# Optimization experiments

Measured on AMD Instinct MI355X. Metric: run time of the kernel, lower is better.

## Reference

```python
import jax, jax.numpy as jnp
import numpy as np
from jax import lax

EPS = 1e-5

def conv2d(x, w, pad):
    return lax.conv_general_dilated(x, w, (1, 1), [(pad, pad), (pad, pad)],
                                    dimension_numbers=('NCHW', 'OIHW', 'NCHW'))

def bn(x, g, b, m, v):
    scale = (g / jnp.sqrt(v + EPS))[None, :, None, None]
    return (x - m[None, :, None, None]) * scale + b[None, :, None, None]

def upsample_bilinear_align_corners(x, scale):
    b, c, h, w = x.shape
    oh, ow = h * scale, w * scale
    ys = jnp.linspace(0.0, h - 1.0, oh)
    xs = jnp.linspace(0.0, w - 1.0, ow)
    y0 = jnp.floor(ys).astype(jnp.int32); y1 = jnp.minimum(y0 + 1, h - 1)
    x0 = jnp.floor(xs).astype(jnp.int32); x1 = jnp.minimum(x0 + 1, w - 1)
    wy = (ys - y0)[None, None, :, None]
    wx = (xs - x0)[None, None, None, :]
    rows = x[:, :, y0, :] * (1.0 - wy) + x[:, :, y1, :] * wy   # (b,c,oh,w)
    return rows[:, :, :, x0] * (1.0 - wx) + rows[:, :, :, x1] * wx

def setup_inputs() -> dict:
    key = jax.random.key(0)
    ks = jax.random.split(key, 12)
    Cin, C4, C8, NC = 2048, 512, 256, 19
    B, H, W = 4, 32, 32
    s = lambda fan: 1.0 / np.sqrt(fan)
    inp = {
        'x': jax.random.normal(ks[0], (B, Cin, H, W), dtype=jnp.float32),
        'conv1_w': jax.random.normal(ks[1], (C4, Cin, 3, 3), jnp.float32) * s(Cin * 9),
        'bn1_g': jnp.ones((C4,)), 'bn1_b': jnp.zeros((C4,)),
        'bn1_m': jnp.zeros((C4,)), 'bn1_v': jnp.ones((C4,)),
        'conv2_w': jax.random.normal(ks[2], (C4, Cin, 3, 3), jnp.float32) * s(Cin * 9),
        'bn2_g': jnp.ones((C4,)), 'bn2_b': jnp.zeros((C4,)),
        'bn2_m': jnp.zeros((C4,)), 'bn2_v': jnp.ones((C4,)),
        'pa_convB_w': jax.random.normal(ks[3], (C4, C4, 1, 1), jnp.float32) * s(C4),
        'pa_gamma': jnp.zeros((1,)),
        'ca_beta': jnp.zeros((1,)),
        'conv3_w': jax.random.normal(ks[4], (C4, C4, 3, 3), jnp.float32) * s(C4 * 9),
        'bn3_g': jnp.ones((C4,)), 'bn3_b': jnp.zeros((C4,)),
        'bn3_m': jnp.zeros((C4,)), 'bn3_v': jnp.ones((C4,)),
        'conv4a_w': jax.random.normal(ks[5], (C8, C4, 3, 3), jnp.float32) * s(C4 * 9),
        'bn4_g': jnp.ones((C8,)), 'bn4_b': jnp.zeros((C8,)),
        'bn4_m': jnp.zeros((C8,)), 'bn4_v': jnp.ones((C8,)),
        'conv4b_w': jax.random.normal(ks[6], (NC, C8, 3, 3), jnp.float32) * s(C8 * 9),
    }
    return inp

def position_attention(x, convB_w, gamma):
    b, c, h, w = x.shape
    # NOTE: original code uses convB for B, C and D (convC/convD unused) - faithful.
    Bm = conv2d(x, convB_w, 0).reshape(b, c, h * w)          # (b,c,hw)
    S = jax.nn.softmax(jnp.einsum('bcn,bcm->bnm', Bm, Bm), axis=-1)  # (b,hw,hw)
    E = jnp.einsum('bcm,bnm->bcn', Bm, S).reshape(b, c, h, w)
    return gamma * E + x

def channel_attention(x, beta):
    b, c, h, w = x.shape
    xf = x.reshape(b, c, h * w)
    A = jax.nn.softmax(jnp.einsum('bcn,bdn->bcd', xf, xf), axis=-1)  # (b,c,c)
    X = jnp.einsum('bkc,bkn->bcn', A, xf).reshape(b, c, h, w)        # A^T @ xf
    return beta * X + x

def reference(x, conv1_w, bn1_g, bn1_b, bn1_m, bn1_v,
              conv2_w, bn2_g, bn2_b, bn2_m, bn2_v,
              pa_convB_w, pa_gamma, ca_beta,
              conv3_w, bn3_g, bn3_b, bn3_m, bn3_v,
              conv4a_w, bn4_g, bn4_b, bn4_m, bn4_v, conv4b_w):
    x_pa = jax.nn.relu(bn(conv2d(x, conv1_w, 1), bn1_g, bn1_b, bn1_m, bn1_v))
    x_ca = jax.nn.relu(bn(conv2d(x, conv2_w, 1), bn2_g, bn2_b, bn2_m, bn2_v))
    pa = position_attention(x_pa, pa_convB_w, pa_gamma)
    ca = channel_attention(x_ca, ca_beta)
    out = jax.nn.relu(bn(conv2d(pa + ca, conv3_w, 1), bn3_g, bn3_b, bn3_m, bn3_v))
    out = upsample_bilinear_align_corners(out, 8)
    out = jax.nn.relu(bn(conv2d(out, conv4a_w, 1), bn4_g, bn4_b, bn4_m, bn4_v))
    out = conv2d(out, conv4b_w, 1)
    return out
```

## Files before the change

### kernel.cpp

```cpp
#include <hip/hip_runtime.h>
#include <stdint.h>

typedef __bf16 v8bf __attribute__((ext_vector_type(8)));
typedef float  v4f  __attribute__((ext_vector_type(4)));

#define MFMA16(a,b,c) __builtin_amdgcn_mfma_f32_16x16x32_bf16((a),(b),(c),0,0,0)

__device__ __forceinline__ void g2l16(void* lds, const void* g) {
  __builtin_amdgcn_global_load_lds(
      (__attribute__((address_space(1))) unsigned int*)g,
      (__attribute__((address_space(3))) unsigned int*)lds, 16, 0, 0);
}


__global__ void bnprep(const float* __restrict__ g, const float* __restrict__ b,
                       const float* __restrict__ m, const float* __restrict__ v,
                       float* __restrict__ sc, float* __restrict__ bi, int C) {
  int i = blockIdx.x * 256 + threadIdx.x;
  if (i < C) {
    float s = g[i] * rsqrtf(v[i] + 1e-5f);
    sc[i] = s;
    bi[i] = b[i] - m[i] * s;
  }
}

__global__ void pack_w(const float* __restrict__ src, __bf16* __restrict__ dst,
                       int co_cnt, int co_src, int co_off, int co_tot, int ci, int taps) {
  int idx = blockIdx.x * 256 + threadIdx.x;
  if (idx >= co_cnt * ci) return;
  int c = idx % ci, co = idx / ci;
  for (int t = 0; t < taps; ++t) {
    float v = (co < co_src) ? src[((size_t)co * ci + c) * taps + t] : 0.f;
    dst[((size_t)t * co_tot + co_off + co) * ci + c] = (__bf16)v;
  }
}

__global__ void cast_x_k(const float* __restrict__ x, __bf16* __restrict__ xb) {
  __shared__ float tl[64][65];
  int p0 = blockIdx.x * 64, c0 = blockIdx.y * 64, n = blockIdx.z;
  const float* xin = x + (size_t)n * 2048 * 1024;
  for (int it = 0; it < 16; ++it) {
    int idx = it * 256 + threadIdx.x;
    int px = idx & 63, cl = idx >> 6;
    tl[px][cl] = xin[(size_t)(c0 + cl) * 1024 + p0 + px];
  }
  __syncthreads();
  for (int it = 0; it < 16; ++it) {
    int idx = it * 256 + threadIdx.x;
    int cl = idx & 63, px = idx >> 6;
    xb[((size_t)n * 1024 + p0 + px) * 2048 + c0 + cl] = (__bf16)tl[px][cl];
  }
}

__global__ void trans_y2(const __bf16* __restrict__ y12, __bf16* __restrict__ y2t) {
  __shared__ __bf16 tl[64][72];
  int p0 = blockIdx.x * 64, c0 = blockIdx.y * 64, n = blockIdx.z;
  for (int it = 0; it < 16; ++it) {
    int idx = it * 256 + threadIdx.x;
    int cl = idx & 63, px = idx >> 6;
    tl[px][cl] = y12[((size_t)n * 1024 + p0 + px) * 1024 + 512 + c0 + cl];
  }
  __syncthreads();
  for (int it = 0; it < 16; ++it) {
    int idx = it * 256 + threadIdx.x;
    int px = idx & 63, cl = idx >> 6;
    y2t[((size_t)n * 512 + c0 + cl) * 1024 + p0 + px] = tl[px][cl];
  }
}

__global__ __launch_bounds__(256, 2)
void gemm_nt(const __bf16* __restrict__ A, const __bf16* __restrict__ B,
             size_t aB, size_t bB, int lda, int ldb, int kch, int mode,
             void* __restrict__ out, void* __restrict__ out2, size_t oB, int ldo) {
  __shared__ __align__(16) __bf16 tile[2][4 * 128 * 8];
  const int tid = threadIdx.x;
  const int lane = tid & 63, wv = tid >> 6;
  const int ln = lane & 15, q = lane >> 4;
  const int wm = wv >> 1, wn = wv & 1;
  const int p0 = blockIdx.x * 128, mb = blockIdx.y * 128, z = blockIdx.z;
  A += (size_t)z * aB; B += (size_t)z * bB;

  v4f acc[4][4];
#pragma unroll
  for (int mf = 0; mf < 4; ++mf)
#pragma unroll
    for (int nf = 0; nf < 4; ++nf)
#pragma unroll
      for (int r = 0; r < 4; ++r) acc[mf][nf][r] = 0.f;

  const __bf16* pa[4];
#pragma unroll
  for (int mf = 0; mf < 4; ++mf)
    pa[mf] = A + (size_t)(mb + wm * 64 + mf * 16 + ln) * lda + q * 8;

#pragma unroll
  for (int t2 = 0; t2 < 2; ++t2)
    g2l16(&tile[0][(wv * 128 + t2 * 64) * 8],
          B + (size_t)(p0 + t2 * 64 + lane) * ldb + wv * 8);
  __syncthreads();

  for (int kc = 0; kc < kch; ++kc) {
    const int tb = kc & 1;
    if (kc + 1 < kch) {
      const int c1 = (kc + 1) * 32;
#pragma unroll
      for (int t2 = 0; t2 < 2; ++t2)
        g2l16(&tile[tb ^ 1][(wv * 128 + t2 * 64) * 8],
              B + (size_t)(p0 + t2 * 64 + lane) * ldb + c1 + wv * 8);
    }
    const int c0 = kc * 32;
    v8bf bfr[4];
#pragma unroll
    for (int nf = 0; nf < 4; ++nf)
      bfr[nf] = *(const v8bf*)&tile[tb][(q * 128 + wn * 64 + nf * 16 + ln) * 8];
#pragma unroll
    for (int mf = 0; mf < 4; ++mf) {
      v8bf af = *(const v8bf*)(pa[mf] + c0);
#pragma unroll
      for (int nf = 0; nf < 4; ++nf)
        acc[mf][nf] = MFMA16(af, bfr[nf], acc[mf][nf]);
    }
    __syncthreads();
  }

#pragma unroll
  for (int mf = 0; mf < 4; ++mf) {
    const int m_l = wm * 64 + mf * 16 + q * 4;
#pragma unroll
    for (int nf = 0; nf < 4; ++nf) {
      const int n_l = wn * 64 + nf * 16 + ln;
      const int P = p0 + n_l;
      if (mode == 1) {
        float* o = (float*)out + (size_t)z * oB;
#pragma unroll
        for (int r = 0; r < 4; ++r)
          o[(size_t)(mb + m_l + r) * ldo + P] = acc[mf][nf][r];
      } else if (mode == 3) {
        float* o = (float*)out + (size_t)z * oB;
        v4f v;
#pragma unroll
        for (int r = 0; r < 4; ++r) v[r] = acc[mf][nf][r];
        *(v4f*)(o + (size_t)P * ldo + mb + m_l) = v;
      } else {
        __bf16* o = (__bf16*)out + (size_t)z * oB;
        union { __bf16 h[4]; uint2 u; } pk;
#pragma unroll
        for (int r = 0; r < 4; ++r) pk.h[r] = (__bf16)acc[mf][nf][r];
        *(uint2*)(o + (size_t)P * ldo + mb + m_l) = pk.u;
        if (mode == 2) {
          __bf16* o2 = (__bf16*)out2 + (size_t)z * oB;
#pragma unroll
          for (int r = 0; r < 4; ++r)
            o2[(size_t)(mb + m_l + r) * 1024 + P] = pk.h[r];
        }
      }
    }
  }
}

template <int CI, int KCH, int KS>
__global__ __launch_bounds__(256, 4)
void conv3x3_sk(const __bf16* __restrict__ in, const __bf16* __restrict__ wp,
                float* __restrict__ part, const int CO) {
  __shared__ __align__(16) __bf16 tile[2][816 * 8];
  const int tid = threadIdx.x;
  const int lane = tid & 63, wv = tid >> 6;
  const int ln = lane & 15, q = lane >> 4;
  const int pblk = blockIdx.x, cb = blockIdx.y, ks = blockIdx.z;
  const int n = pblk >> 3, y0 = (pblk & 7) << 2;
  const int wm = wv >> 1, wn = wv & 1;
  const int KCN = KCH / KS;
  const int kbase = ks * KCN;

  for (int t = tid; t < 1632; t += 256) ((uint4*)tile)[t] = make_uint4(0, 0, 0, 0);

  v4f acc[4][4];
#pragma unroll
  for (int mf = 0; mf < 4; ++mf)
#pragma unroll
    for (int nf = 0; nf < 4; ++nf)
#pragma unroll
      for (int r = 0; r < 4; ++r) acc[mf][nf][r] = 0.f;

  const __bf16* pa[4];
#pragma unroll
  for (int mf = 0; mf < 4; ++mf) {
    int co = cb * 128 + wm * 64 + mf * 16 + ln;
    pa[mf] = wp + (size_t)co * CI + kbase * 32 + q * 8;
  }
  int pixb[4];
#pragma unroll
  for (int nf = 0; nf < 4; ++nf) {
    int n_l = wn * 64 + nf * 16 + ln;
    pixb[nf] = (n_l >> 5) * 34 + (n_l & 31);
  }
  const __bf16* inb = in + (size_t)n * 1024 * CI + kbase * 32;
  __syncthreads();

  if (lane < 32) {
#pragma unroll
    for (int t2 = 0; t2 < 6; ++t2) {
      int y = y0 - 1 + t2;
      if (y >= 0 && y < 32)
        g2l16(&tile[0][(wv * 204 + t2 * 34 + 1) * 8],
              inb + ((size_t)(y * 32 + lane) * CI + wv * 8));
    }
  }
  __syncthreads();

  for (int kc = 0; kc < KCN; ++kc) {
    const int tb = kc & 1;
    if (kc + 1 < KCN && lane < 32) {
      const int c1 = (kc + 1) * 32;
#pragma unroll
      for (int t2 = 0; t2 < 6; ++t2) {
        int y = y0 - 1 + t2;
        if (y >= 0 && y < 32)
          g2l16(&tile[tb ^ 1][(wv * 204 + t2 * 34 + 1) * 8],
                inb + ((size_t)(y * 32 + lane) * CI + c1 + wv * 8));
      }
    }
    const int ci0 = kc * 32;
#pragma unroll
    for (int tap = 0; tap < 9; ++tap) {
      const int ty = tap / 3, tx = tap % 3;
      v8bf bfr[4];
#pragma unroll
      for (int nf = 0; nf < 4; ++nf)
        bfr[nf] = *(const v8bf*)&tile[tb][(q * 204 + pixb[nf] + ty * 34 + tx) * 8];
      const size_t toff = (size_t)tap * CO * CI + ci0;
#pragma unroll
      for (int mf = 0; mf < 4; ++mf) {
        v8bf af = *(const v8bf*)(pa[mf] + toff);
#pragma unroll
        for (int nf = 0; nf < 4; ++nf)
          acc[mf][nf] = MFMA16(af, bfr[nf], acc[mf][nf]);
      }
    }
    __syncthreads();
  }

  float* po = part + ((size_t)ks * 4096 + (size_t)n * 1024) * CO;
#pragma unroll
  for (int mf = 0; mf < 4; ++mf) {
    const int m_l = wm * 64 + mf * 16 + q * 4;
#pragma unroll
    for (int nf = 0; nf < 4; ++nf) {
      const int n_l = wn * 64 + nf * 16 + ln;
      const int p_img = (y0 + (n_l >> 5)) * 32 + (n_l & 31);
      *(v4f*)(po + (size_t)p_img * CO + cb * 128 + m_l) = acc[mf][nf];
    }
  }
}

template <int CO, int KS>
__global__ __launch_bounds__(256, 8)
void reduce_bn_relu(const float* __restrict__ part, const float* __restrict__ sc,
                    const float* __restrict__ bi, __bf16* __restrict__ out) {
  const size_t splitStride = (size_t)4096 * CO;
  size_t gi = (size_t)blockIdx.x * 256 + threadIdx.x;
  size_t row = gi / (CO / 4);
  int c4 = (int)(gi % (CO / 4)) * 4;
  const float* p = part + row * CO + c4;
  v4f a = *(const v4f*)p;
#pragma unroll
  for (int s = 1; s < KS; ++s) {
    v4f b = *(const v4f*)(p + s * splitStride);
#pragma unroll
    for (int r = 0; r < 4; ++r) a[r] += b[r];
  }
  const v4f s4 = *(const v4f*)(sc + c4);
  const v4f b4 = *(const v4f*)(bi + c4);
  union { __bf16 h[4]; uint2 u; } pk;
#pragma unroll
  for (int r = 0; r < 4; ++r)
    pk.h[r] = (__bf16)fmaxf(a[r] * s4[r] + b4[r], 0.f);
  *(uint2*)(out + row * CO + c4) = pk.u;
}

__global__ __launch_bounds__(256, 4)
void up_combine(const float* __restrict__ D, const float* __restrict__ sc,
                const float* __restrict__ bi, __bf16* __restrict__ y4) {
  const int tid = threadIdx.x;
  const int coq = blockIdx.x;
  const int oy = blockIdx.y;
  const int n = blockIdx.z;
  const int co = coq * 64 + (tid & 15) * 4;
  const int px0 = (tid >> 4) * 16;

  const v4f s4 = *(const v4f*)(sc + co);
  const v4f b4 = *(const v4f*)(bi + co);

  v4f acc[16];
#pragma unroll
  for (int j = 0; j < 16; ++j)
#pragma unroll
    for (int r = 0; r < 4; ++r) acc[j][r] = 0.f;

  const float* Dn = D + (size_t)n * 1024 * 2304;

#pragma unroll
  for (int ty = 0; ty < 3; ++ty) {
    int fy = oy + ty - 1;
    if (fy < 0 || fy > 255) continue;
    float syf = fy * (31.0f / 255.0f);
    int rA = (int)syf; float wy = syf - rA;
    int rB = rA < 31 ? rA + 1 : 31;
    float wA = 1.f - wy, wB = wy;
    const float* rowA = Dn + (size_t)rA * 32 * 2304;
    const float* rowB = Dn + (size_t)rB * 32 * 2304;
#pragma unroll
    for (int tx = 0; tx < 3; ++tx) {
      const int tco = (ty * 3 + tx) * 256 + co;
      int cur = -99;
      v4f a0{}, a1{}, b0{}, b1{};
#pragma unroll
      for (int j = 0; j < 16; ++j) {
        int fx = px0 + j + tx - 1;
        if (fx < 0 || fx > 255) continue;
        float sxf = fx * (31.0f / 255.0f);
        int c0 = (int)sxf; float wx = sxf - c0;
        if (c0 != cur) {
          cur = c0;
          int c1 = c0 < 31 ? c0 + 1 : 31;
          a0 = *(const v4f*)(rowA + (size_t)c0 * 2304 + tco);
          a1 = *(const v4f*)(rowA + (size_t)c1 * 2304 + tco);
          b0 = *(const v4f*)(rowB + (size_t)c0 * 2304 + tco);
          b1 = *(const v4f*)(rowB + (size_t)c1 * 2304 + tco);
        }
        float wxA = 1.f - wx;
        float cA = wA * wxA, cB = wA * wx, cC = wB * wxA, cD = wB * wx;
#pragma unroll
        for (int r = 0; r < 4; ++r)
          acc[j][r] += cA * a0[r] + cB * a1[r] + cC * b0[r] + cD * b1[r];
      }
    }
  }

  __bf16* ob = y4 + (((size_t)n * 65536 + (size_t)oy * 256 + px0) * 256 + co);
#pragma unroll
  for (int j = 0; j < 16; ++j) {
    union { __bf16 h[4]; uint2 u; } pk;
#pragma unroll
    for (int r = 0; r < 4; ++r) {
      float v = acc[j][r] * s4[r] + b4[r];
      pk.h[r] = (__bf16)fmaxf(v, 0.f);
    }
    *(uint2*)(ob + (size_t)j * 256) = pk.u;
  }
}

__global__ __launch_bounds__(256, 4)
void conv4b_k(const __bf16* __restrict__ y4, const __bf16* __restrict__ wp,
              float* __restrict__ outp) {
  __shared__ __align__(16) __bf16 tile[2][816 * 8];
  const int tid = threadIdx.x;
  const int lane = tid & 63, wv = tid >> 6;
  const int ln = lane & 15, q = lane >> 4;
  const int xblk = blockIdx.x, strip = blockIdx.y, n = blockIdx.z;
  const int oy0 = strip * 4, ox0 = xblk * 32;

  for (int t = tid; t < 1632; t += 256) ((uint4*)tile)[t] = make_uint4(0, 0, 0, 0);

  v4f acc[2][2];
#pragma unroll
  for (int mf = 0; mf < 2; ++mf)
#pragma unroll
    for (int nf = 0; nf < 2; ++nf)
#pragma unroll
      for (int r = 0; r < 4; ++r) acc[mf][nf][r] = 0.f;

  const __bf16* pa[2];
#pragma unroll
  for (int mf = 0; mf < 2; ++mf)
    pa[mf] = wp + (size_t)(mf * 16 + ln) * 256 + q * 8;
  int pixb[2];
#pragma unroll
  for (int nf = 0; nf < 2; ++nf) {
    int n_l = wv * 32 + nf * 16 + ln;
    pixb[nf] = (n_l >> 5) * 34 + (n_l & 31);
  }
  const __bf16* src = y4 + (size_t)n * 65536 * 256;
  const int gx = ox0 - 1 + lane;
  const bool xin = (lane < 34) && (gx >= 0) && (gx < 256);
  __syncthreads();

#pragma unroll
  for (int t2 = 0; t2 < 6; ++t2) {
    int y = oy0 - 1 + t2;
    if (y >= 0 && y < 256 && xin)
      g2l16(&tile[0][(wv * 204 + t2 * 34) * 8],
            src + ((size_t)(y * 256 + gx) * 256 + wv * 8));
  }
  __syncthreads();

  for (int kc = 0; kc < 8; ++kc) {
    const int tb = kc & 1;
    if (kc + 1 < 8) {
      const int c1 = (kc + 1) * 32;
#pragma unroll
      for (int t2 = 0; t2 < 6; ++t2) {
        int y = oy0 - 1 + t2;
        if (y >= 0 && y < 256 && xin)
          g2l16(&tile[tb ^ 1][(wv * 204 + t2 * 34) * 8],
                src + ((size_t)(y * 256 + gx) * 256 + c1 + wv * 8));
      }
    }
    const int ci0 = kc * 32;
#pragma unroll
    for (int tap = 0; tap < 9; ++tap) {
      const int ty = tap / 3, tx = tap % 3;
      v8bf bfr[2];
#pragma unroll
      for (int nf = 0; nf < 2; ++nf)
        bfr[nf] = *(const v8bf*)&tile[tb][(q * 204 + pixb[nf] + ty * 34 + tx) * 8];
      const size_t toff = (size_t)tap * 32 * 256 + ci0;
#pragma unroll
      for (int mf = 0; mf < 2; ++mf) {
        v8bf af = *(const v8bf*)(pa[mf] + toff);
#pragma unroll
        for (int nf = 0; nf < 2; ++nf)
          acc[mf][nf] = MFMA16(af, bfr[nf], acc[mf][nf]);
      }
    }
    __syncthreads();
  }

#pragma unroll
  for (int mf = 0; mf < 2; ++mf) {
    const int m_l = mf * 16 + q * 4;
#pragma unroll
    for (int nf = 0; nf < 2; ++nf) {
      const int n_l = wv * 32 + nf * 16 + ln;
      const int oy = oy0 + (n_l >> 5), ox = ox0 + (n_l & 31);
#pragma unroll
      for (int r = 0; r < 4; ++r) {
        int co = m_l + r;
        if (co < 19)
          outp[(((size_t)n * 19 + co) * 256 + oy) * 256 + ox] = acc[mf][nf][r];
      }
    }
  }
}


__global__ void softmax1024(const float* __restrict__ S, __bf16* __restrict__ O) {
  __shared__ float red[256];
  const int row = blockIdx.x, tid = threadIdx.x;
  const float* p = S + (size_t)row * 1024;
  float v0 = p[tid], v1 = p[tid + 256], v2 = p[tid + 512], v3 = p[tid + 768];
  float m = fmaxf(fmaxf(v0, v1), fmaxf(v2, v3));
  red[tid] = m; __syncthreads();
  for (int s = 128; s > 0; s >>= 1) { if (tid < s) red[tid] = fmaxf(red[tid], red[tid + s]); __syncthreads(); }
  m = red[0]; __syncthreads();
  v0 = __expf(v0 - m); v1 = __expf(v1 - m); v2 = __expf(v2 - m); v3 = __expf(v3 - m);
  red[tid] = v0 + v1 + v2 + v3; __syncthreads();
  for (int s = 128; s > 0; s >>= 1) { if (tid < s) red[tid] += red[tid + s]; __syncthreads(); }
  float inv = 1.0f / red[0];
  __bf16* o = O + (size_t)row * 1024;
  o[tid] = (__bf16)(v0 * inv); o[tid + 256] = (__bf16)(v1 * inv);
  o[tid + 512] = (__bf16)(v2 * inv); o[tid + 768] = (__bf16)(v3 * inv);
}

__global__ void softmaxT512(const float* __restrict__ S, __bf16* __restrict__ O) {
  __shared__ float red[256];
  const int row = blockIdx.x, tid = threadIdx.x;
  const float* p = S + (size_t)row * 512;
  float v0 = p[tid], v1 = p[tid + 256];
  float m = fmaxf(v0, v1);
  red[tid] = m; __syncthreads();
  for (int s = 128; s > 0; s >>= 1) { if (tid < s) red[tid] = fmaxf(red[tid], red[tid + s]); __syncthreads(); }
  m = red[0]; __syncthreads();
  v0 = __expf(v0 - m); v1 = __expf(v1 - m);
  red[tid] = v0 + v1; __syncthreads();
  for (int s = 128; s > 0; s >>= 1) { if (tid < s) red[tid] += red[tid + s]; __syncthreads(); }
  float inv = 1.0f / red[0];
  int n = row >> 9, c = row & 511;
  __bf16* o = O + (size_t)n * 262144 + c;
  o[(size_t)tid * 512] = (__bf16)(v0 * inv);
  o[(size_t)(tid + 256) * 512] = (__bf16)(v1 * inv);
}

__global__ void combine_z(const __bf16* __restrict__ y12, const __bf16* __restrict__ E,
                          const __bf16* __restrict__ X, const float* __restrict__ gp,
                          const float* __restrict__ bp, __bf16* __restrict__ z) {
  size_t i = (size_t)blockIdx.x * 256 + threadIdx.x;
  int pg = (int)(i >> 9), c = (int)(i & 511);
  float g = gp[0], b = bp[0];
  float v = (float)y12[(size_t)pg * 1024 + c] + (float)y12[(size_t)pg * 1024 + 512 + c] +
            g * (float)E[i] + b * (float)X[i];
  z[i] = (__bf16)v;
}


extern "C" void kernel_launch(void* const* d_in, const int* in_sizes, int n_in,
                              void* d_out, int out_size, void* d_ws, size_t ws_size,
                              hipStream_t stream) {
  const float* x    = (const float*)d_in[0];
  const float* w1   = (const float*)d_in[1];
  const float* bn1g = (const float*)d_in[2];
  const float* bn1b = (const float*)d_in[3];
  const float* bn1m = (const float*)d_in[4];
  const float* bn1v = (const float*)d_in[5];
  const float* w2   = (const float*)d_in[6];
  const float* bn2g = (const float*)d_in[7];
  const float* bn2b = (const float*)d_in[8];
  const float* bn2m = (const float*)d_in[9];
  const float* bn2v = (const float*)d_in[10];
  const float* wB   = (const float*)d_in[11];
  const float* gam  = (const float*)d_in[12];
  const float* bet  = (const float*)d_in[13];
  const float* w3   = (const float*)d_in[14];
  const float* bn3g = (const float*)d_in[15];
  const float* bn3b = (const float*)d_in[16];
  const float* bn3m = (const float*)d_in[17];
  const float* bn3v = (const float*)d_in[18];
  const float* w4a  = (const float*)d_in[19];
  const float* bn4g = (const float*)d_in[20];
  const float* bn4b = (const float*)d_in[21];
  const float* bn4m = (const float*)d_in[22];
  const float* bn4v = (const float*)d_in[23];
  const float* w4b  = (const float*)d_in[24];

  char* ws = (char*)d_ws;
  size_t off = 0;
  auto take = [&](size_t bytes) -> char* {
    char* p = ws + off;
    off += (bytes + 255) & ~(size_t)255;
    return p;
  };
  __bf16* w12b  = (__bf16*)take(9ULL * 1024 * 2048 * 2);
  __bf16* w3b   = (__bf16*)take(9ULL * 512 * 512 * 2);
  __bf16* w4ab  = (__bf16*)take(9ULL * 256 * 512 * 2);
  __bf16* w4bb  = (__bf16*)take(9ULL * 32 * 256 * 2);
  __bf16* wBb   = (__bf16*)take(512ULL * 512 * 2);
  float*  sc12  = (float*)take(1024 * 4);
  float*  bi12  = (float*)take(1024 * 4);
  float*  sc3   = (float*)take(512 * 4);
  float*  bi3   = (float*)take(512 * 4);
  float*  sc4   = (float*)take(256 * 4);
  float*  bi4   = (float*)take(256 * 4);
  __bf16* xb    = (__bf16*)take(4ULL * 1024 * 2048 * 2);
  __bf16* y12   = (__bf16*)take(4ULL * 1024 * 1024 * 2);
  __bf16* Bm_pc = (__bf16*)take(4ULL * 1024 * 512 * 2);
  __bf16* Bm_cp = (__bf16*)take(4ULL * 512 * 1024 * 2);
  float*  Smat  = (float*)take(4ULL * 1024 * 1024 * 4);
  __bf16* Ssm   = (__bf16*)take(4ULL * 1024 * 1024 * 2);
  __bf16* E_pc  = (__bf16*)take(4ULL * 1024 * 512 * 2);
  __bf16* y2t   = (__bf16*)take(4ULL * 512 * 1024 * 2);
  float*  Scc   = (float*)take(4ULL * 512 * 512 * 4);
  __bf16* AsmT  = (__bf16*)take(4ULL * 512 * 512 * 2);
  __bf16* X_pc  = (__bf16*)take(4ULL * 1024 * 512 * 2);
  __bf16* zb    = (__bf16*)take(4ULL * 1024 * 512 * 2);
  __bf16* y4    = (__bf16*)take(4ULL * 65536 * 256 * 2);
  __bf16* y3    = (__bf16*)take(4ULL * 1024 * 512 * 2);
  float* Dmat = (float*)xb;
  float* partK = (float*)y4;

  bnprep<<<2, 256, 0, stream>>>(bn1g, bn1b, bn1m, bn1v, sc12, bi12, 512);
  bnprep<<<2, 256, 0, stream>>>(bn2g, bn2b, bn2m, bn2v, sc12 + 512, bi12 + 512, 512);
  bnprep<<<2, 256, 0, stream>>>(bn3g, bn3b, bn3m, bn3v, sc3, bi3, 512);
  bnprep<<<1, 256, 0, stream>>>(bn4g, bn4b, bn4m, bn4v, sc4, bi4, 256);
  pack_w<<<4096, 256, 0, stream>>>(w1, w12b, 512, 512, 0, 1024, 2048, 9);
  pack_w<<<4096, 256, 0, stream>>>(w2, w12b, 512, 512, 512, 1024, 2048, 9);
  pack_w<<<1024, 256, 0, stream>>>(w3, w3b, 512, 512, 0, 512, 512, 9);
  pack_w<<<512, 256, 0, stream>>>(w4a, w4ab, 256, 256, 0, 256, 512, 9);
  pack_w<<<32, 256, 0, stream>>>(w4b, w4bb, 32, 19, 0, 32, 256, 9);
  pack_w<<<1024, 256, 0, stream>>>(wB, wBb, 512, 512, 0, 512, 512, 1);
  cast_x_k<<<dim3(16, 32, 4), 256, 0, stream>>>(x, xb);

  conv3x3_sk<2048, 64, 4><<<dim3(32, 8, 4), 256, 0, stream>>>(xb, w12b, partK, 1024);
  reduce_bn_relu<1024, 4><<<4096, 256, 0, stream>>>(partK, sc12, bi12, y12);

  gemm_nt<<<dim3(8, 4, 4), 256, 0, stream>>>(wBb, y12, 0, 1048576, 512, 1024, 16, 2,
                                             Bm_pc, Bm_cp, 524288, 512);
  gemm_nt<<<dim3(8, 8, 4), 256, 0, stream>>>(Bm_pc, Bm_pc, 524288, 524288, 512, 512, 16, 1,
                                             Smat, nullptr, 1048576, 1024);
  softmax1024<<<4096, 256, 0, stream>>>(Smat, Ssm);
  gemm_nt<<<dim3(8, 4, 4), 256, 0, stream>>>(Bm_cp, Ssm, 524288, 1048576, 1024, 1024, 32, 0,
                                             E_pc, nullptr, 524288, 512);

  trans_y2<<<dim3(16, 8, 4), 256, 0, stream>>>(y12, y2t);
  gemm_nt<<<dim3(4, 4, 4), 256, 0, stream>>>(y2t, y2t, 524288, 524288, 1024, 1024, 32, 1,
                                             Scc, nullptr, 262144, 512);
  softmaxT512<<<2048, 256, 0, stream>>>(Scc, AsmT);
  gemm_nt<<<dim3(8, 4, 4), 256, 0, stream>>>(AsmT, y12 + 512, 262144, 1048576, 512, 1024, 16, 0,
                                             X_pc, nullptr, 524288, 512);

  combine_z<<<8192, 256, 0, stream>>>(y12, E_pc, X_pc, gam, bet, zb);

  conv3x3_sk<512, 16, 4><<<dim3(32, 4, 4), 256, 0, stream>>>(zb, w3b, partK, 512);
  reduce_bn_relu<512, 4><<<2048, 256, 0, stream>>>(partK, sc3, bi3, y3);

  gemm_nt<<<dim3(8, 18, 4), 256, 0, stream>>>(w4ab, y3, 0, 524288, 512, 512, 16, 3,
                                              Dmat, nullptr, 2359296, 2304);
  up_combine<<<dim3(4, 256, 4), 256, 0, stream>>>(Dmat, sc4, bi4, y4);

  conv4b_k<<<dim3(8, 64, 4), 256, 0, stream>>>(y4, w4bb, (float*)d_out);
}
```

Baseline: 1.301 ms.

## Register-prefetch weight fragments in conv and GEMM loops; reorder conv grid

```diff
diff --git a/kernel.cpp b/kernel.cpp
--- a/kernel.cpp
+++ b/kernel.cpp
@@ -97,6 +97,9 @@
   for (int t2 = 0; t2 < 2; ++t2)
     g2l16(&tile[0][(wv * 128 + t2 * 64) * 8],
           B + (size_t)(p0 + t2 * 64 + lane) * ldb + wv * 8);
+  v8bf acur[4];
+#pragma unroll
+  for (int mf = 0; mf < 4; ++mf) acur[mf] = *(const v8bf*)(pa[mf]);
   __syncthreads();
 
   for (int kc = 0; kc < kch; ++kc) {
@@ -108,18 +111,22 @@
         g2l16(&tile[tb ^ 1][(wv * 128 + t2 * 64) * 8],
               B + (size_t)(p0 + t2 * 64 + lane) * ldb + c1 + wv * 8);
     }
-    const int c0 = kc * 32;
+    v8bf anxt[4];
+#pragma unroll
+    for (int mf = 0; mf < 4; ++mf)
+      anxt[mf] = *(const v8bf*)(pa[mf] + (kc + 1) * 32);
     v8bf bfr[4];
 #pragma unroll
     for (int nf = 0; nf < 4; ++nf)
       bfr[nf] = *(const v8bf*)&tile[tb][(q * 128 + wn * 64 + nf * 16 + ln) * 8];
 #pragma unroll
     for (int mf = 0; mf < 4; ++mf) {
-      v8bf af = *(const v8bf*)(pa[mf] + c0);
 #pragma unroll
       for (int nf = 0; nf < 4; ++nf)
-        acc[mf][nf] = MFMA16(af, bfr[nf], acc[mf][nf]);
-    }
+        acc[mf][nf] = MFMA16(acur[mf], bfr[nf], acc[mf][nf]);
+    }
+#pragma unroll
+    for (int mf = 0; mf < 4; ++mf) acur[mf] = anxt[mf];
     __syncthreads();
   }
 
@@ -159,18 +166,19 @@
 }
 
 template <int CI, int KCH, int KS>
-__global__ __launch_bounds__(256, 4)
+__global__ __launch_bounds__(256, 3)
 void conv3x3_sk(const __bf16* __restrict__ in, const __bf16* __restrict__ wp,
                 float* __restrict__ part, const int CO) {
   __shared__ __align__(16) __bf16 tile[2][816 * 8];
   const int tid = threadIdx.x;
   const int lane = tid & 63, wv = tid >> 6;
   const int ln = lane & 15, q = lane >> 4;
-  const int pblk = blockIdx.x, cb = blockIdx.y, ks = blockIdx.z;
+  const int cb = blockIdx.x, pblk = blockIdx.y, ks = blockIdx.z;
   const int n = pblk >> 3, y0 = (pblk & 7) << 2;
   const int wm = wv >> 1, wn = wv & 1;
   const int KCN = KCH / KS;
   const int kbase = ks * KCN;
+  const size_t WT = (size_t)CO * CI;
 
   for (int t = tid; t < 1632; t += 256) ((uint4*)tile)[t] = make_uint4(0, 0, 0, 0);
 
@@ -206,6 +214,11 @@
               inb + ((size_t)(y * 32 + lane) * CI + wv * 8));
     }
   }
+  v8bf wcur[4], wnx1[4];
+#pragma unroll
+  for (int mf = 0; mf < 4; ++mf) wcur[mf] = *(const v8bf*)(pa[mf]);
+#pragma unroll
+  for (int mf = 0; mf < 4; ++mf) wnx1[mf] = *(const v8bf*)(pa[mf] + WT);
   __syncthreads();
 
   for (int kc = 0; kc < KCN; ++kc) {
@@ -220,22 +233,27 @@
                 inb + ((size_t)(y * 32 + lane) * CI + c1 + wv * 8));
       }
     }
-    const int ci0 = kc * 32;
 #pragma unroll
     for (int tap = 0; tap < 9; ++tap) {
       const int ty = tap / 3, tx = tap % 3;
+      const int nt = (tap + 2) % 9;
+      const int nkc = kc + (tap + 2) / 9;
+      v8bf wnew[4];
+#pragma unroll
+      for (int mf = 0; mf < 4; ++mf)
+        wnew[mf] = *(const v8bf*)(pa[mf] + (size_t)nt * WT + nkc * 32);
       v8bf bfr[4];
 #pragma unroll
       for (int nf = 0; nf < 4; ++nf)
         bfr[nf] = *(const v8bf*)&tile[tb][(q * 204 + pixb[nf] + ty * 34 + tx) * 8];
-      const size_t toff = (size_t)tap * CO * CI + ci0;
 #pragma unroll
       for (int mf = 0; mf < 4; ++mf) {
-        v8bf af = *(const v8bf*)(pa[mf] + toff);
 #pragma unroll
         for (int nf = 0; nf < 4; ++nf)
-          acc[mf][nf] = MFMA16(af, bfr[nf], acc[mf][nf]);
+          acc[mf][nf] = MFMA16(wcur[mf], bfr[nf], acc[mf][nf]);
       }
+#pragma unroll
+      for (int mf = 0; mf < 4; ++mf) { wcur[mf] = wnx1[mf]; wnx1[mf] = wnew[mf]; }
     }
     __syncthreads();
   }
@@ -359,6 +377,7 @@
   const int ln = lane & 15, q = lane >> 4;
   const int xblk = blockIdx.x, strip = blockIdx.y, n = blockIdx.z;
   const int oy0 = strip * 4, ox0 = xblk * 32;
+  const size_t WT = (size_t)32 * 256;
 
   for (int t = tid; t < 1632; t += 256) ((uint4*)tile)[t] = make_uint4(0, 0, 0, 0);
 
@@ -392,6 +411,11 @@
       g2l16(&tile[0][(wv * 204 + t2 * 34) * 8],
             src + ((size_t)(y * 256 + gx) * 256 + wv * 8));
   }
+  v8bf wcur[2], wnx1[2];
+#pragma unroll
+  for (int mf = 0; mf < 2; ++mf) wcur[mf] = *(const v8bf*)(pa[mf]);
+#pragma unroll
+  for (int mf = 0; mf < 2; ++mf) wnx1[mf] = *(const v8bf*)(pa[mf] + WT);
   __syncthreads();
 
   for (int kc = 0; kc < 8; ++kc) {
@@ -406,22 +430,27 @@
                 src + ((size_t)(y * 256 + gx) * 256 + c1 + wv * 8));
       }
     }
-    const int ci0 = kc * 32;
 #pragma unroll
     for (int tap = 0; tap < 9; ++tap) {
       const int ty = tap / 3, tx = tap % 3;
+      const int nt = (tap + 2) % 9;
+      const int nkc = kc + (tap + 2) / 9;
+      v8bf wnew[2];
+#pragma unroll
+      for (int mf = 0; mf < 2; ++mf)
+        wnew[mf] = *(const v8bf*)(pa[mf] + (size_t)nt * WT + nkc * 32);
       v8bf bfr[2];
 #pragma unroll
       for (int nf = 0; nf < 2; ++nf)
         bfr[nf] = *(const v8bf*)&tile[tb][(q * 204 + pixb[nf] + ty * 34 + tx) * 8];
-      const size_t toff = (size_t)tap * 32 * 256 + ci0;
 #pragma unroll
       for (int mf = 0; mf < 2; ++mf) {
-        v8bf af = *(const v8bf*)(pa[mf] + toff);
 #pragma unroll
         for (int nf = 0; nf < 2; ++nf)
-          acc[mf][nf] = MFMA16(af, bfr[nf], acc[mf][nf]);
+          acc[mf][nf] = MFMA16(wcur[mf], bfr[nf], acc[mf][nf]);
       }
+#pragma unroll
+      for (int mf = 0; mf < 2; ++mf) { wcur[mf] = wnx1[mf]; wnx1[mf] = wnew[mf]; }
     }
     __syncthreads();
   }
@@ -569,7 +598,7 @@
   pack_w<<<1024, 256, 0, stream>>>(wB, wBb, 512, 512, 0, 512, 512, 1);
   cast_x_k<<<dim3(16, 32, 4), 256, 0, stream>>>(x, xb);
 
-  conv3x3_sk<2048, 64, 4><<<dim3(32, 8, 4), 256, 0, stream>>>(xb, w12b, partK, 1024);
+  conv3x3_sk<2048, 64, 4><<<dim3(8, 32, 4), 256, 0, stream>>>(xb, w12b, partK, 1024);
   reduce_bn_relu<1024, 4><<<4096, 256, 0, stream>>>(partK, sc12, bi12, y12);
 
   gemm_nt<<<dim3(8, 4, 4), 256, 0, stream>>>(wBb, y12, 0, 1048576, 512, 1024, 16, 2,
@@ -589,7 +618,7 @@
 
   combine_z<<<8192, 256, 0, stream>>>(y12, E_pc, X_pc, gam, bet, zb);
 
-  conv3x3_sk<512, 16, 4><<<dim3(32, 4, 4), 256, 0, stream>>>(zb, w3b, partK, 512);
+  conv3x3_sk<512, 16, 4><<<dim3(4, 32, 4), 256, 0, stream>>>(zb, w3b, partK, 512);
   reduce_bn_relu<512, 4><<<2048, 256, 0, stream>>>(partK, sc3, bi3, y3);
 
   gemm_nt<<<dim3(8, 18, 4), 256, 0, stream>>>(w4ab, y3, 0, 524288, 512, 512, 16, 3,
```

New measurement: 1.316 ms. No clear change (+1.2%).
